# Kernel tuning notes

Hardware: AMD Instinct MI355X
Metric: run time of the kernel (lower is better)

Reference implementation:

```python
import jax, jax.numpy as jnp
import numpy as np

D_MODEL = 1024
EXPAND = 2
D_INNER = D_MODEL * EXPAND  # 2048
D_STATE = 16
D_CONV = 4
DT_RANK = (D_MODEL + 15) // 16  # 64
BATCH = 2
SEQ = 1024


def setup_inputs() -> dict:
    key = jax.random.key(0)
    ks = jax.random.split(key, 10)
    s = lambda d: 1.0 / np.sqrt(d)
    x = jax.random.normal(ks[0], (BATCH, SEQ, D_MODEL), dtype=jnp.float32)
    W_in = jax.random.normal(ks[1], (D_MODEL, 2 * D_INNER), dtype=jnp.float32) * s(D_MODEL)
    conv_w = jax.random.normal(ks[2], (D_INNER, D_CONV), dtype=jnp.float32) * s(D_CONV)
    conv_b = jax.random.normal(ks[3], (D_INNER,), dtype=jnp.float32) * 0.02
    W_x = jax.random.normal(ks[4], (D_INNER, DT_RANK + 2 * D_STATE), dtype=jnp.float32) * s(D_INNER)
    W_dt = jax.random.normal(ks[5], (DT_RANK, D_INNER), dtype=jnp.float32) * s(DT_RANK)
    b_dt = jax.random.uniform(ks[6], (D_INNER,), dtype=jnp.float32, minval=-4.0, maxval=-2.0)
    # S4D-real init: A = -[1..d_state] per channel
    A_log = jnp.log(jnp.tile(jnp.arange(1, D_STATE + 1, dtype=jnp.float32), (D_INNER, 1)))
    D = jnp.ones((D_INNER,), dtype=jnp.float32)
    W_out = jax.random.normal(ks[7], (D_INNER, D_MODEL), dtype=jnp.float32) * s(D_INNER)
    return {"x": x, "W_in": W_in, "conv_w": conv_w, "conv_b": conv_b,
            "W_x": W_x, "W_dt": W_dt, "b_dt": b_dt, "A_log": A_log,
            "D": D, "W_out": W_out}


def _mamba_forward(x, W_in, conv_w, conv_b, W_x, W_dt, b_dt, A_log, D, W_out):
    B, L, _ = x.shape
    # input projection -> [B, L, 2*d_inner], split into u (conv branch) and z (gate)
    xz = jnp.einsum('bld,de->ble', x, W_in)
    u, z = jnp.split(xz, 2, axis=-1)  # each [B, L, d_inner]

    # causal depthwise conv over time
    u_c = jnp.transpose(u, (0, 2, 1))                      # [B, d_inner, L]
    u_c = jnp.pad(u_c, ((0, 0), (0, 0), (D_CONV - 1, 0)))  # left pad for causality
    kern = conv_w[:, None, :]                              # [d_inner, 1, d_conv]
    u_c = jax.lax.conv_general_dilated(
        u_c, kern, window_strides=(1,), padding='VALID',
        dimension_numbers=('NCH', 'OIH', 'NCH'),
        feature_group_count=D_INNER)
    u_c = u_c + conv_b[None, :, None]
    u_c = jax.nn.silu(jnp.transpose(u_c, (0, 2, 1)))       # [B, L, d_inner]

    # data-dependent SSM parameters
    x_dbl = jnp.einsum('bld,de->ble', u_c, W_x)            # [B, L, dt_rank+2*d_state]
    dt_lowrank = x_dbl[..., :DT_RANK]
    Bmat = x_dbl[..., DT_RANK:DT_RANK + D_STATE]           # [B, L, d_state]
    Cmat = x_dbl[..., DT_RANK + D_STATE:]                  # [B, L, d_state]
    dt = jax.nn.softplus(jnp.einsum('blr,rd->bld', dt_lowrank, W_dt) + b_dt)

    A = -jnp.exp(A_log)                                    # [d_inner, d_state]

    # selective scan over time: h' = exp(dt*A) h + dt*B*u ; y = <h, C>
    def step(h, inp):
        u_t, dt_t, B_t, C_t = inp                          # [B,d], [B,d], [B,n], [B,n]
        dA = jnp.exp(dt_t[..., None] * A)                  # [B, d_inner, d_state]
        dBu = (dt_t * u_t)[..., None] * B_t[:, None, :]    # [B, d_inner, d_state]
        h = dA * h + dBu
        y_t = jnp.einsum('bdn,bn->bd', h, C_t)
        return h, y_t

    h0 = jnp.zeros((B, D_INNER, D_STATE), dtype=x.dtype)
    seq = (jnp.swapaxes(u_c, 0, 1), jnp.swapaxes(dt, 0, 1),
           jnp.swapaxes(Bmat, 0, 1), jnp.swapaxes(Cmat, 0, 1))
    _, ys = jax.lax.scan(step, h0, seq)                    # ys: [L, B, d_inner]
    y = jnp.swapaxes(ys, 0, 1) + u_c * D                   # skip term
    y = y * jax.nn.silu(z)                                 # gate
    return jnp.einsum('bld,de->ble', y, W_out)             # [B, L, d_model]


def reference(x, W_in, conv_w, conv_b, W_x, W_dt, b_dt, A_log, D, W_out):
    return _mamba_forward(x, W_in, conv_w, conv_b, W_x, W_dt, b_dt, A_log, D, W_out)
```

## Files before the change

kernel.cpp:

```cpp
#include <hip/hip_runtime.h>
#include <hip/hip_bf16.h>


typedef __attribute__((ext_vector_type(8))) short bfrag;
typedef __attribute__((ext_vector_type(4))) float f32x4;

#define CF   32
#define CLEN 32

__device__ __forceinline__ unsigned short f2bf(float f) {
    unsigned int u = __float_as_uint(f);
    u += 0x7FFF + ((u >> 16) & 1);
    return (unsigned short)(u >> 16);
}
__device__ __forceinline__ float bf2f(unsigned short s) {
    return __uint_as_float((unsigned int)s << 16);
}

__device__ __forceinline__ void async_copy16(const unsigned short* g,
                                             unsigned short* l) {
    __builtin_amdgcn_global_load_lds(
        (const __attribute__((address_space(1))) void*)g,
        (__attribute__((address_space(3))) void*)l, 16, 0, 0);
}

template<int MT, int NT>
__global__ __launch_bounds__(256) void gemm_bf16_v2(
    const unsigned short* __restrict__ A,
    const unsigned short* __restrict__ BT,
    float* __restrict__ C,
    unsigned short* __restrict__ C1,
    int K, int lda, int ldb, int ldc, int split)
{
    constexpr int FI  = MT / 32;
    constexpr int FJ  = NT / 32;
    constexpr int ACH = MT / 32;
    constexpr int BCH = NT / 32;
    __shared__ __align__(16) unsigned short sA[MT * 64];
    __shared__ __align__(16) unsigned short sB[NT * 64];

    const int tid  = threadIdx.x;
    const int wave = tid >> 6, lane = tid & 63;
    const int lm   = lane & 15;
    const int quad = lane >> 4;
    const int wrow = (wave >> 1) * (MT / 2);
    const int wcol = (wave & 1) * (NT / 2);
    const int bm = blockIdx.y * MT, bn = blockIdx.x * NT;

    const int lrow = lane >> 3;
    const int lkb  = (lane & 7) ^ lrow;

    f32x4 acc[FI][FJ];
    #pragma unroll
    for (int i = 0; i < FI; ++i)
        #pragma unroll
        for (int j = 0; j < FJ; ++j) {
            acc[i][j][0] = 0.f; acc[i][j][1] = 0.f;
            acc[i][j][2] = 0.f; acc[i][j][3] = 0.f;
        }

    for (int k0 = 0; k0 < K; k0 += 64) {
        #pragma unroll
        for (int c = 0; c < ACH; ++c) {
            const int chunk = wave * ACH + c;
            const int row = chunk * 8 + lrow;
            async_copy16(&A[(size_t)(bm + row) * lda + k0 + lkb * 8],
                         &sA[chunk * 512 + lane * 8]);
        }
        #pragma unroll
        for (int c = 0; c < BCH; ++c) {
            const int chunk = wave * BCH + c;
            const int row = chunk * 8 + lrow;
            async_copy16(&BT[(size_t)(bn + row) * ldb + k0 + lkb * 8],
                         &sB[chunk * 512 + lane * 8]);
        }
        __syncthreads();

        #pragma unroll
        for (int ks = 0; ks < 2; ++ks) {
            bfrag af[FI], bf[FJ];
            #pragma unroll
            for (int i = 0; i < FI; ++i) {
                const int row = wrow + i * 16 + lm;
                const int slot = (ks * 4 + quad) ^ (row & 7);
                af[i] = *(const bfrag*)&sA[row * 64 + slot * 8];
            }
            #pragma unroll
            for (int j = 0; j < FJ; ++j) {
                const int row = wcol + j * 16 + lm;
                const int slot = (ks * 4 + quad) ^ (row & 7);
                bf[j] = *(const bfrag*)&sB[row * 64 + slot * 8];
            }
            #pragma unroll
            for (int i = 0; i < FI; ++i)
                #pragma unroll
                for (int j = 0; j < FJ; ++j)
                    acc[i][j] = __builtin_amdgcn_mfma_f32_16x16x32_bf16(
                        af[i], bf[j], acc[i][j], 0, 0, 0);
        }
        __syncthreads();
    }

    #pragma unroll
    for (int i = 0; i < FI; ++i)
        #pragma unroll
        for (int j = 0; j < FJ; ++j) {
            const int col = bn + wcol + j * 16 + lm;
            #pragma unroll
            for (int r = 0; r < 4; ++r) {
                const int row = bm + wrow + i * 16 + quad * 4 + r;
                float v = acc[i][j][r];
                if (split > 0) {
                    if (col < split) C [(size_t)row * split + col] = v;
                    else             C1[(size_t)row * split + (col - split)] = f2bf(v);
                } else {
                    C[(size_t)row * ldc + col] = v;
                }
            }
        }
}

__global__ __launch_bounds__(256) void transpose_cast(
    const float* __restrict__ in, unsigned short* __restrict__ out,
    int rows, int cols)
{
    __shared__ float tile[32][33];
    const int j0 = blockIdx.x * 32, i0 = blockIdx.y * 32;
    const int tx = threadIdx.x & 31, ty = threadIdx.x >> 5;
    #pragma unroll
    for (int k = 0; k < 4; ++k)
        tile[ty + 8 * k][tx] = in[(size_t)(i0 + ty + 8 * k) * cols + j0 + tx];
    __syncthreads();
    #pragma unroll
    for (int k = 0; k < 4; ++k)
        out[(size_t)(j0 + ty + 8 * k) * rows + i0 + tx] = f2bf(tile[tx][ty + 8 * k]);
}

__global__ __launch_bounds__(256) void cast_bf16(
    const float* __restrict__ in, unsigned short* __restrict__ out)
{
    int i = (blockIdx.x * 256 + threadIdx.x) * 4;
    float4 v = *(const float4*)&in[i];
    ushort4 o;
    o.x = f2bf(v.x); o.y = f2bf(v.y); o.z = f2bf(v.z); o.w = f2bf(v.w);
    *(ushort4*)&out[i] = o;
}

#define SK_KS 128
__global__ __launch_bounds__(256) void gemm_f32_splitk(
    const unsigned short* __restrict__ A,
    const float* __restrict__ B,
    float* __restrict__ part)
{
    __shared__ __align__(16) float As[16][64];
    __shared__ __align__(16) float Bs[16][96];

    const int tid = threadIdx.x;
    const int mtile = blockIdx.x >> 4;
    const int kslice = blockIdx.x & 15;
    const int bm = mtile * 64;
    const int kbase = kslice * SK_KS;

    const int am = tid >> 2;
    const int ak = (tid & 3) << 2;

    const int ty = tid >> 4, tx = tid & 15;
    const int rm = ty << 2;
    const int rn = tx * 6;

    float acc[4][6] = {};

    for (int k0 = 0; k0 < SK_KS; k0 += 16) {
        ushort4 av = *(const ushort4*)&A[(size_t)(bm + am) * 2048 + kbase + k0 + ak];
        As[ak + 0][am] = bf2f(av.x);
        As[ak + 1][am] = bf2f(av.y);
        As[ak + 2][am] = bf2f(av.z);
        As[ak + 3][am] = bf2f(av.w);
        for (int i = tid; i < 384; i += 256) {
            int br = i / 24, bc = (i % 24) << 2;
            *(float4*)&Bs[br][bc] = *(const float4*)&B[(size_t)(kbase + k0 + br) * 96 + bc];
        }
        __syncthreads();

        #pragma unroll
        for (int k = 0; k < 16; ++k) {
            float4 a = *(const float4*)&As[k][rm];
            float b[6];
            #pragma unroll
            for (int j = 0; j < 6; ++j) b[j] = Bs[k][rn + j];
            #pragma unroll
            for (int j = 0; j < 6; ++j) {
                acc[0][j] += a.x * b[j];
                acc[1][j] += a.y * b[j];
                acc[2][j] += a.z * b[j];
                acc[3][j] += a.w * b[j];
            }
        }
        __syncthreads();
    }

    float* pout = part + (size_t)kslice * 196608;
    #pragma unroll
    for (int i = 0; i < 4; ++i) {
        float* crow = pout + (size_t)(bm + rm + i) * 96 + rn;
        #pragma unroll
        for (int j = 0; j < 6; ++j)
            crow[j] = acc[i][j];
    }
}

__global__ __launch_bounds__(256) void reduce_splitk(
    const float* __restrict__ part, float* __restrict__ xdbl)
{
    int i = (blockIdx.x * 256 + threadIdx.x) * 4;
    float4 acc = {0.f, 0.f, 0.f, 0.f};
    #pragma unroll
    for (int s = 0; s < 16; ++s) {
        float4 v = *(const float4*)&part[(size_t)s * 196608 + i];
        acc.x += v.x; acc.y += v.y; acc.z += v.z; acc.w += v.w;
    }
    *(float4*)&xdbl[i] = acc;
}

#define BM 64
#define BN 64
#define BK 16
__global__ __launch_bounds__(256) void gemm_f32(
    const float* __restrict__ A, const float* __restrict__ B,
    float* __restrict__ C, int M, int N, int K,
    int lda, int ldb, int ldc, int mode, const float* __restrict__ bias)
{
    __shared__ __align__(16) float As[BK][BM];
    __shared__ __align__(16) float Bs[BK][BN];

    const int tid = threadIdx.x;
    const int bm = blockIdx.y * BM;
    const int bn = blockIdx.x * BN;

    const int am = tid >> 2;
    const int ak = (tid & 3) << 2;
    const int bk = tid >> 4;
    const int bnn = (tid & 15) << 2;

    const int tx = tid & 15, ty = tid >> 4;
    const int rm = ty << 2;
    const int rn = tx << 2;
    const int cm = bm + rm, cn = bn + rn;

    float acc[4][4] = {};

    for (int k0 = 0; k0 < K; k0 += BK) {
        const float* ap = A + (size_t)(bm + am) * lda + (k0 + ak);
        float4 av = *(const float4*)ap;
        As[ak + 0][am] = av.x;
        As[ak + 1][am] = av.y;
        As[ak + 2][am] = av.z;
        As[ak + 3][am] = av.w;
        {
            const int ncol = bn + bnn;
            const float* bp = B + (size_t)(k0 + bk) * ldb + ncol;
            float4 bv;
            if (ncol + 3 < N) {
                bv = *(const float4*)bp;
            } else {
                bv.x = (ncol + 0 < N) ? bp[0] : 0.f;
                bv.y = (ncol + 1 < N) ? bp[1] : 0.f;
                bv.z = (ncol + 2 < N) ? bp[2] : 0.f;
                bv.w = (ncol + 3 < N) ? bp[3] : 0.f;
            }
            *(float4*)&Bs[bk][bnn] = bv;
        }
        __syncthreads();

        #pragma unroll
        for (int k = 0; k < BK; ++k) {
            float4 a = *(const float4*)&As[k][rm];
            float4 b = *(const float4*)&Bs[k][rn];
            acc[0][0] += a.x * b.x; acc[0][1] += a.x * b.y;
            acc[0][2] += a.x * b.z; acc[0][3] += a.x * b.w;
            acc[1][0] += a.y * b.x; acc[1][1] += a.y * b.y;
            acc[1][2] += a.y * b.z; acc[1][3] += a.y * b.w;
            acc[2][0] += a.z * b.x; acc[2][1] += a.z * b.y;
            acc[2][2] += a.z * b.z; acc[2][3] += a.z * b.w;
            acc[3][0] += a.w * b.x; acc[3][1] += a.w * b.y;
            acc[3][2] += a.w * b.z; acc[3][3] += a.w * b.w;
        }
        __syncthreads();
    }

    #pragma unroll
    for (int i = 0; i < 4; ++i) {
        #pragma unroll
        for (int j = 0; j < 4; ++j) {
            int col = cn + j;
            if (col < N) {
                float v = acc[i][j];
                if (mode == 1) {
                    v += bias[col];
                    v = (v > 20.f) ? v : logf(1.f + expf(v));
                    ((unsigned short*)C)[(size_t)(cm + i) * ldc + col] = f2bf(v);
                } else {
                    C[(size_t)(cm + i) * ldc + col] = v;
                }
            }
        }
    }
}

__global__ __launch_bounds__(256) void conv_silu_kernel(
    const float* __restrict__ upre, const float* __restrict__ cw,
    const float* __restrict__ cb, unsigned short* __restrict__ uc)
{
    int idx = blockIdx.x * 256 + threadIdx.x;
    int d = idx & 2047;
    int r = idx >> 11;
    int l = r & 1023;

    float4 w4 = *(const float4*)(cw + 4 * d);
    float w[4] = { w4.x, w4.y, w4.z, w4.w };
    float acc = cb[d];
    const float* up = upre + (size_t)r * 2048 + d;
    if (l >= 3) {
        acc += w[0] * up[-3 * 2048] + w[1] * up[-2 * 2048]
             + w[2] * up[-1 * 2048] + w[3] * up[0];
    } else {
        #pragma unroll
        for (int j = 0; j < 4; ++j) {
            int lj = l - 3 + j;
            if (lj >= 0) acc += w[j] * up[(j - 3) * 2048];
        }
    }
    float sig = 1.f / (1.f + expf(-acc));
    uc[idx] = f2bf(acc * sig);
}

__global__ __launch_bounds__(256) void scan_pass1(
    const unsigned short* __restrict__ uc,
    const unsigned short* __restrict__ dtb,
    const float* __restrict__ xdbl,
    const float* __restrict__ A_log,
    float* __restrict__ Hend,
    float* __restrict__ Sdt)
{
    __shared__ float sB[CLEN][16];
    const int tid = threadIdx.x;
    const int bx  = blockIdx.x;
    const int c   = bx & (CF - 1);
    const int g   = (bx >> 5) & 7;
    const int b   = bx >> 8;
    const int d   = g * 256 + tid;
    const size_t rowbase = (size_t)b * 1024 + c * CLEN;

    for (int i = tid; i < CLEN * 16; i += 256) {
        int tt = i >> 4, nn = i & 15;
        sB[tt][nn] = xdbl[(rowbase + tt) * 96 + 64 + nn];
    }

    float A2[16];
    {
        float al[16];
        #pragma unroll
        for (int q = 0; q < 4; ++q)
            *(float4*)&al[4 * q] = *(const float4*)&A_log[(size_t)d * 16 + 4 * q];
        #pragma unroll
        for (int n = 0; n < 16; ++n) A2[n] = -expf(al[n]) * 1.44269504f;
    }
    __syncthreads();

    float h[16];
    #pragma unroll
    for (int n = 0; n < 16; ++n) h[n] = 0.f;
    float sdt = 0.f;

    #pragma unroll 4
    for (int t = 0; t < CLEN; ++t) {
        size_t r = rowbase + t;
        float dtv = bf2f(dtb[r * 2048 + d]);
        float uv  = bf2f(uc [r * 2048 + d]);
        sdt += dtv;
        float dtu = dtv * uv;
        float bl[16];
        #pragma unroll
        for (int q = 0; q < 4; ++q)
            *(float4*)&bl[4 * q] = *(const float4*)&sB[t][4 * q];
        #pragma unroll
        for (int n = 0; n < 16; ++n)
            h[n] = exp2f(dtv * A2[n]) * h[n] + dtu * bl[n];
    }

    size_t base = ((size_t)(b * CF + c) * 2048 + d) * 16;
    #pragma unroll
    for (int q = 0; q < 4; ++q)
        *(float4*)&Hend[base + 4 * q] = *(float4*)&h[4 * q];
    Sdt[(size_t)(b * CF + c) * 2048 + d] = sdt;
}

__global__ __launch_bounds__(256) void scan_pass2(
    const float* __restrict__ Hend, const float* __restrict__ Sdt,
    const float* __restrict__ A_log, float* __restrict__ Hin)
{
    int gid = blockIdx.x * 256 + threadIdx.x;
    int b = gid >> 15;
    int rest = gid & 32767;
    int d = rest >> 4;
    float A2 = -expf(A_log[rest]) * 1.44269504f;
    float H = 0.f;
    #pragma unroll
    for (int c = 0; c < CF; ++c) {
        size_t sidx = (size_t)(b * CF + c) * 2048 + d;
        size_t idx  = ((size_t)(b * CF + c) << 15) + rest;
        Hin[idx] = H;
        H = exp2f(A2 * Sdt[sidx]) * H + Hend[idx];
    }
}

__global__ __launch_bounds__(256) void scan_pass3(
    const unsigned short* __restrict__ uc,
    const unsigned short* __restrict__ dtb,
    const unsigned short* __restrict__ zb,
    const float* __restrict__ xdbl,
    const float* __restrict__ A_log,
    const float* __restrict__ Dvec,
    const float* __restrict__ Hin,
    unsigned short* __restrict__ yb)
{
    __shared__ float sBC[CLEN][32];
    const int tid = threadIdx.x;
    const int bx  = blockIdx.x;
    const int c   = bx & (CF - 1);
    const int g   = (bx >> 5) & 7;
    const int b   = bx >> 8;
    const int d   = g * 256 + tid;
    const size_t rowbase = (size_t)b * 1024 + c * CLEN;

    for (int i = tid; i < CLEN * 32; i += 256) {
        int tt = i >> 5, j = i & 31;
        sBC[tt][j] = xdbl[(rowbase + tt) * 96 + 64 + j];
    }

    float A2[16];
    {
        float al[16];
        #pragma unroll
        for (int q = 0; q < 4; ++q)
            *(float4*)&al[4 * q] = *(const float4*)&A_log[(size_t)d * 16 + 4 * q];
        #pragma unroll
        for (int n = 0; n < 16; ++n) A2[n] = -expf(al[n]) * 1.44269504f;
    }
    const float Dd = Dvec[d];

    float h[16];
    {
        size_t base = ((size_t)(b * CF + c) * 2048 + d) * 16;
        #pragma unroll
        for (int q = 0; q < 4; ++q)
            *(float4*)&h[4 * q] = *(const float4*)&Hin[base + 4 * q];
    }
    __syncthreads();

    #pragma unroll 2
    for (int t = 0; t < CLEN; ++t) {
        size_t r = rowbase + t;
        float dtv = bf2f(dtb[r * 2048 + d]);
        float uv  = bf2f(uc [r * 2048 + d]);
        float zv  = bf2f(zb [r * 2048 + d]);
        float dtu = dtv * uv;
        float bl[16], cl[16];
        #pragma unroll
        for (int q = 0; q < 4; ++q) {
            *(float4*)&bl[4 * q] = *(const float4*)&sBC[t][4 * q];
            *(float4*)&cl[4 * q] = *(const float4*)&sBC[t][16 + 4 * q];
        }
        float acc = uv * Dd;
        #pragma unroll
        for (int n = 0; n < 16; ++n) {
            h[n] = exp2f(dtv * A2[n]) * h[n] + dtu * bl[n];
            acc += h[n] * cl[n];
        }
        float yv = acc * zv / (1.f + expf(-zv));
        yb[r * 2048 + d] = f2bf(yv);
    }
}

extern "C" void kernel_launch(void* const* d_in, const int* in_sizes, int n_in,
                              void* d_out, int out_size, void* d_ws, size_t ws_size,
                              hipStream_t stream)
{
    const float* x      = (const float*)d_in[0];
    const float* W_in   = (const float*)d_in[1];
    const float* conv_w = (const float*)d_in[2];
    const float* conv_b = (const float*)d_in[3];
    const float* W_x    = (const float*)d_in[4];
    const float* W_dt   = (const float*)d_in[5];
    const float* b_dt   = (const float*)d_in[6];
    const float* A_log  = (const float*)d_in[7];
    const float* Dv     = (const float*)d_in[8];
    const float* W_out  = (const float*)d_in[9];
    float* out = (float*)d_out;

    float* ws    = (float*)d_ws;
    float* upre  = ws;
    unsigned short* dtb = (unsigned short*)upre;
    unsigned short* uc = (unsigned short*)(ws + 4194304);
    float* xdbl  = ws + 4194304 + 2097152;
    float* Hend  = xdbl + 196608;
    float* Hin   = Hend + 2097152;
    float* Sdt   = Hin + 2097152;
    float* part  = Hend;
    unsigned short* zb   = (unsigned short*)(Sdt + 131072);
    unsigned short* xb   = zb + 4194304;
    unsigned short* wbT  = xb + 2097152;
    unsigned short* wobT = wbT + 4194304;
    unsigned short* yb   = wbT;

    dim3 blk(256);

    transpose_cast<<<dim3(128, 32), blk, 0, stream>>>(W_in, wbT, 1024, 4096);
    transpose_cast<<<dim3(32, 64), blk, 0, stream>>>(W_out, wobT, 2048, 1024);
    cast_bf16<<<2048, blk, 0, stream>>>(x, xb);

    gemm_bf16_v2<128, 128><<<dim3(32, 16), blk, 0, stream>>>(
        xb, wbT, upre, zb, 1024, 1024, 1024, 0, 2048);

    conv_silu_kernel<<<(2048 * 2048) / 256, blk, 0, stream>>>(upre, conv_w, conv_b, uc);

    gemm_f32_splitk<<<512, blk, 0, stream>>>(uc, W_x, part);
    reduce_splitk<<<192, blk, 0, stream>>>(part, xdbl);

    gemm_f32<<<dim3(32, 32), blk, 0, stream>>>(
        xdbl, W_dt, (float*)dtb, 2048, 2048, 64, 96, 2048, 2048, 1, b_dt);

    scan_pass1<<<512, blk, 0, stream>>>(uc, dtb, xdbl, A_log, Hend, Sdt);
    scan_pass2<<<256, blk, 0, stream>>>(Hend, Sdt, A_log, Hin);
    scan_pass3<<<512, blk, 0, stream>>>(uc, dtb, zb, xdbl, A_log, Dv, Hin, yb);

    gemm_bf16_v2<64, 64><<<dim3(16, 32), blk, 0, stream>>>(
        yb, wobT, out, nullptr, 2048, 2048, 2048, 1024, 0);
}
```

Before: 271.8 us.

## Fuse prep kernels, store u in bf16, move dt projection to MFMA GEMM

Merges the three weight and input conversion kernels into one launch, which also transposes W_dt to bf16. The input projection now writes the u branch as bf16 instead of fp32, which halves that traffic, and its tile shape changes to 128x64. The reduce step also emits a bf16 copy of the dt-rank slice, so the dt projection with bias and softplus runs on the bf16 MFMA GEMM instead of the scalar fp32 GEMM. This lowers launch count and memory traffic, at the cost of extra bf16 rounding on u and the dt inputs.

```diff
diff --git a/kernel.cpp b/kernel.cpp
--- a/kernel.cpp
+++ b/kernel.cpp
@@ -29,8 +29,10 @@
     const unsigned short* __restrict__ A,
     const unsigned short* __restrict__ BT,
     float* __restrict__ C,
-    unsigned short* __restrict__ C1,
-    int K, int lda, int ldb, int ldc, int split)
+    unsigned short* __restrict__ Cb0,
+    unsigned short* __restrict__ Cb1,
+    int K, int lda, int ldb, int ldc, int split,
+    const float* __restrict__ bias)
 {
     constexpr int FI  = MT / 32;
     constexpr int FJ  = NT / 32;
@@ -110,9 +112,13 @@
             for (int r = 0; r < 4; ++r) {
                 const int row = bm + wrow + i * 16 + quad * 4 + r;
                 float v = acc[i][j][r];
-                if (split > 0) {
-                    if (col < split) C [(size_t)row * split + col] = v;
-                    else             C1[(size_t)row * split + (col - split)] = f2bf(v);
+                if (bias != nullptr) {
+                    v += bias[col];
+                    v = (v > 20.f) ? v : logf(1.f + expf(v));
+                    Cb0[(size_t)row * ldc + col] = f2bf(v);
+                } else if (split > 0) {
+                    if (col < split) Cb0[(size_t)row * split + col] = f2bf(v);
+                    else             Cb1[(size_t)row * split + (col - split)] = f2bf(v);
                 } else {
                     C[(size_t)row * ldc + col] = v;
                 }
@@ -120,13 +126,33 @@
         }
 }
 
-__global__ __launch_bounds__(256) void transpose_cast(
-    const float* __restrict__ in, unsigned short* __restrict__ out,
-    int rows, int cols)
+__global__ __launch_bounds__(256) void prep_fused(
+    const float* __restrict__ W_in, const float* __restrict__ W_out,
+    const float* __restrict__ W_dt, const float* __restrict__ x,
+    unsigned short* __restrict__ wbT, unsigned short* __restrict__ wobT,
+    unsigned short* __restrict__ wdtT, unsigned short* __restrict__ xb)
 {
     __shared__ float tile[32][33];
-    const int j0 = blockIdx.x * 32, i0 = blockIdx.y * 32;
-    const int tx = threadIdx.x & 31, ty = threadIdx.x >> 5;
+    const int bx = blockIdx.x;
+    const int tid = threadIdx.x;
+
+    const float* in; unsigned short* out; int rows, cols, jt, it;
+    if (bx < 4096)      { in = W_in;  out = wbT;  rows = 1024; cols = 4096;
+                          jt = bx & 127; it = bx >> 7; }
+    else if (bx < 6144) { int t = bx - 4096; in = W_out; out = wobT;
+                          rows = 2048; cols = 1024; jt = t & 31; it = t >> 5; }
+    else if (bx < 6272) { int t = bx - 6144; in = W_dt;  out = wdtT;
+                          rows = 64;   cols = 2048; jt = t & 63; it = t >> 6; }
+    else {
+        int i = ((bx - 6272) * 256 + tid) * 4;
+        float4 v = *(const float4*)&x[i];
+        ushort4 o;
+        o.x = f2bf(v.x); o.y = f2bf(v.y); o.z = f2bf(v.z); o.w = f2bf(v.w);
+        *(ushort4*)&xb[i] = o;
+        return;
+    }
+    const int j0 = jt * 32, i0 = it * 32;
+    const int tx = tid & 31, ty = tid >> 5;
     #pragma unroll
     for (int k = 0; k < 4; ++k)
         tile[ty + 8 * k][tx] = in[(size_t)(i0 + ty + 8 * k) * cols + j0 + tx];
@@ -134,16 +160,6 @@
     #pragma unroll
     for (int k = 0; k < 4; ++k)
         out[(size_t)(j0 + ty + 8 * k) * rows + i0 + tx] = f2bf(tile[tx][ty + 8 * k]);
-}
-
-__global__ __launch_bounds__(256) void cast_bf16(
-    const float* __restrict__ in, unsigned short* __restrict__ out)
-{
-    int i = (blockIdx.x * 256 + threadIdx.x) * 4;
-    float4 v = *(const float4*)&in[i];
-    ushort4 o;
-    o.x = f2bf(v.x); o.y = f2bf(v.y); o.z = f2bf(v.z); o.w = f2bf(v.w);
-    *(ushort4*)&out[i] = o;
 }
 
 #define SK_KS 128
@@ -210,7 +226,8 @@
 }
 
 __global__ __launch_bounds__(256) void reduce_splitk(
-    const float* __restrict__ part, float* __restrict__ xdbl)
+    const float* __restrict__ part, float* __restrict__ xdbl,
+    unsigned short* __restrict__ dtl)
 {
     int i = (blockIdx.x * 256 + threadIdx.x) * 4;
     float4 acc = {0.f, 0.f, 0.f, 0.f};
@@ -220,95 +237,17 @@
         acc.x += v.x; acc.y += v.y; acc.z += v.z; acc.w += v.w;
     }
     *(float4*)&xdbl[i] = acc;
-}
-
-#define BM 64
-#define BN 64
-#define BK 16
-__global__ __launch_bounds__(256) void gemm_f32(
-    const float* __restrict__ A, const float* __restrict__ B,
-    float* __restrict__ C, int M, int N, int K,
-    int lda, int ldb, int ldc, int mode, const float* __restrict__ bias)
-{
-    __shared__ __align__(16) float As[BK][BM];
-    __shared__ __align__(16) float Bs[BK][BN];
-
-    const int tid = threadIdx.x;
-    const int bm = blockIdx.y * BM;
-    const int bn = blockIdx.x * BN;
-
-    const int am = tid >> 2;
-    const int ak = (tid & 3) << 2;
-    const int bk = tid >> 4;
-    const int bnn = (tid & 15) << 2;
-
-    const int tx = tid & 15, ty = tid >> 4;
-    const int rm = ty << 2;
-    const int rn = tx << 2;
-    const int cm = bm + rm, cn = bn + rn;
-
-    float acc[4][4] = {};
-
-    for (int k0 = 0; k0 < K; k0 += BK) {
-        const float* ap = A + (size_t)(bm + am) * lda + (k0 + ak);
-        float4 av = *(const float4*)ap;
-        As[ak + 0][am] = av.x;
-        As[ak + 1][am] = av.y;
-        As[ak + 2][am] = av.z;
-        As[ak + 3][am] = av.w;
-        {
-            const int ncol = bn + bnn;
-            const float* bp = B + (size_t)(k0 + bk) * ldb + ncol;
-            float4 bv;
-            if (ncol + 3 < N) {
-                bv = *(const float4*)bp;
-            } else {
-                bv.x = (ncol + 0 < N) ? bp[0] : 0.f;
-                bv.y = (ncol + 1 < N) ? bp[1] : 0.f;
-                bv.z = (ncol + 2 < N) ? bp[2] : 0.f;
-                bv.w = (ncol + 3 < N) ? bp[3] : 0.f;
-            }
-            *(float4*)&Bs[bk][bnn] = bv;
-        }
-        __syncthreads();
-
-        #pragma unroll
-        for (int k = 0; k < BK; ++k) {
-            float4 a = *(const float4*)&As[k][rm];
-            float4 b = *(const float4*)&Bs[k][rn];
-            acc[0][0] += a.x * b.x; acc[0][1] += a.x * b.y;
-            acc[0][2] += a.x * b.z; acc[0][3] += a.x * b.w;
-            acc[1][0] += a.y * b.x; acc[1][1] += a.y * b.y;
-            acc[1][2] += a.y * b.z; acc[1][3] += a.y * b.w;
-            acc[2][0] += a.z * b.x; acc[2][1] += a.z * b.y;
-            acc[2][2] += a.z * b.z; acc[2][3] += a.z * b.w;
-            acc[3][0] += a.w * b.x; acc[3][1] += a.w * b.y;
-            acc[3][2] += a.w * b.z; acc[3][3] += a.w * b.w;
-        }
-        __syncthreads();
-    }
-
-    #pragma unroll
-    for (int i = 0; i < 4; ++i) {
-        #pragma unroll
-        for (int j = 0; j < 4; ++j) {
-            int col = cn + j;
-            if (col < N) {
-                float v = acc[i][j];
-                if (mode == 1) {
-                    v += bias[col];
-                    v = (v > 20.f) ? v : logf(1.f + expf(v));
-                    ((unsigned short*)C)[(size_t)(cm + i) * ldc + col] = f2bf(v);
-                } else {
-                    C[(size_t)(cm + i) * ldc + col] = v;
-                }
-            }
-        }
+    int row = i / 96, col = i % 96;
+    if (col < 64) {
+        ushort4 o;
+        o.x = f2bf(acc.x); o.y = f2bf(acc.y);
+        o.z = f2bf(acc.z); o.w = f2bf(acc.w);
+        *(ushort4*)&dtl[(size_t)row * 64 + col] = o;
     }
 }
 
 __global__ __launch_bounds__(256) void conv_silu_kernel(
-    const float* __restrict__ upre, const float* __restrict__ cw,
+    const unsigned short* __restrict__ ub, const float* __restrict__ cw,
     const float* __restrict__ cb, unsigned short* __restrict__ uc)
 {
     int idx = blockIdx.x * 256 + threadIdx.x;
@@ -319,15 +258,15 @@
     float4 w4 = *(const float4*)(cw + 4 * d);
     float w[4] = { w4.x, w4.y, w4.z, w4.w };
     float acc = cb[d];
-    const float* up = upre + (size_t)r * 2048 + d;
+    const unsigned short* up = ub + (size_t)r * 2048 + d;
     if (l >= 3) {
-        acc += w[0] * up[-3 * 2048] + w[1] * up[-2 * 2048]
-             + w[2] * up[-1 * 2048] + w[3] * up[0];
+        acc += w[0] * bf2f(up[-3 * 2048]) + w[1] * bf2f(up[-2 * 2048])
+             + w[2] * bf2f(up[-1 * 2048]) + w[3] * bf2f(up[0]);
     } else {
         #pragma unroll
         for (int j = 0; j < 4; ++j) {
             int lj = l - 3 + j;
-            if (lj >= 0) acc += w[j] * up[(j - 3) * 2048];
+            if (lj >= 0) acc += w[j] * bf2f(up[(j - 3) * 2048]);
         }
     }
     float sig = 1.f / (1.f + expf(-acc));
@@ -498,42 +437,43 @@
     const float* W_out  = (const float*)d_in[9];
     float* out = (float*)d_out;
 
-    float* ws    = (float*)d_ws;
-    float* upre  = ws;
-    unsigned short* dtb = (unsigned short*)upre;
-    unsigned short* uc = (unsigned short*)(ws + 4194304);
-    float* xdbl  = ws + 4194304 + 2097152;
-    float* Hend  = xdbl + 196608;
-    float* Hin   = Hend + 2097152;
-    float* Sdt   = Hin + 2097152;
-    float* part  = Hend;
+    float* ws = (float*)d_ws;
+    unsigned short* ub  = (unsigned short*)ws;
+    unsigned short* dtb = ub;
+    unsigned short* uc  = ub + 4194304;
+    float* xdbl = ws + 4194304;
+    unsigned short* dtl = (unsigned short*)(xdbl + 196608);
+    float* Hend = xdbl + 196608 + 65536;
+    float* Hin  = Hend + 2097152;
+    float* Sdt  = Hin + 2097152;
+    float* part = Hend;
     unsigned short* zb   = (unsigned short*)(Sdt + 131072);
     unsigned short* xb   = zb + 4194304;
     unsigned short* wbT  = xb + 2097152;
     unsigned short* wobT = wbT + 4194304;
+    unsigned short* wdtT = wobT + 2097152;
     unsigned short* yb   = wbT;
 
     dim3 blk(256);
 
-    transpose_cast<<<dim3(128, 32), blk, 0, stream>>>(W_in, wbT, 1024, 4096);
-    transpose_cast<<<dim3(32, 64), blk, 0, stream>>>(W_out, wobT, 2048, 1024);
-    cast_bf16<<<2048, blk, 0, stream>>>(x, xb);
-
-    gemm_bf16_v2<128, 128><<<dim3(32, 16), blk, 0, stream>>>(
-        xb, wbT, upre, zb, 1024, 1024, 1024, 0, 2048);
-
-    conv_silu_kernel<<<(2048 * 2048) / 256, blk, 0, stream>>>(upre, conv_w, conv_b, uc);
+    prep_fused<<<8320, blk, 0, stream>>>(W_in, W_out, W_dt, x,
+                                         wbT, wobT, wdtT, xb);
+
+    gemm_bf16_v2<128, 64><<<dim3(64, 16), blk, 0, stream>>>(
+        xb, wbT, nullptr, ub, zb, 1024, 1024, 1024, 2048, 2048, nullptr);
+
+    conv_silu_kernel<<<(2048 * 2048) / 256, blk, 0, stream>>>(ub, conv_w, conv_b, uc);
 
     gemm_f32_splitk<<<512, blk, 0, stream>>>(uc, W_x, part);
-    reduce_splitk<<<192, blk, 0, stream>>>(part, xdbl);
-
-    gemm_f32<<<dim3(32, 32), blk, 0, stream>>>(
-        xdbl, W_dt, (float*)dtb, 2048, 2048, 64, 96, 2048, 2048, 1, b_dt);
+    reduce_splitk<<<192, blk, 0, stream>>>(part, xdbl, dtl);
+
+    gemm_bf16_v2<128, 128><<<dim3(16, 16), blk, 0, stream>>>(
+        dtl, wdtT, nullptr, dtb, nullptr, 64, 64, 64, 2048, 0, b_dt);
 
     scan_pass1<<<512, blk, 0, stream>>>(uc, dtb, xdbl, A_log, Hend, Sdt);
     scan_pass2<<<256, blk, 0, stream>>>(Hend, Sdt, A_log, Hin);
     scan_pass3<<<512, blk, 0, stream>>>(uc, dtb, zb, xdbl, A_log, Dv, Hin, yb);
 
     gemm_bf16_v2<64, 64><<<dim3(16, 32), blk, 0, stream>>>(
-        yb, wobT, out, nullptr, 2048, 2048, 2048, 1024, 0);
-}
+        yb, wobT, out, nullptr, nullptr, 2048, 2048, 2048, 1024, 0, nullptr);
+}
```

After: 275.7 us. Within noise of the previous version (+1.5%).
